# Performance work log

Measured on AMD Instinct MI355X. Metric: run time of the kernel, lower is better.

The kernel has to match this reference:

```python
import jax, jax.numpy as jnp
import numpy as np
from jax import lax


def _conv(x, W):
    # NCHW conv, stride 1, SAME padding (padding = kernel//2 in original)
    return lax.conv_general_dilated(x, W, (1, 1), 'SAME',
                                    dimension_numbers=('NCHW', 'OIHW', 'NCHW'))


def _cconv(zr, zi, Wr, Wi, br, bi):
    # complex conv: (zr + i*zi) * (Wr + i*Wi)
    yr = _conv(zr, Wr) - _conv(zi, Wi) + br[None, :, None, None]
    yi = _conv(zr, Wi) + _conv(zi, Wr) + bi[None, :, None, None]
    return yr, yi


def setup_inputs() -> dict:
    key = jax.random.key(0)
    B, C, H, W = 16, 128, 64, 64        # C = 128 total = 64 real + 64 imag channels
    half = C // 2                        # 64 complex channels
    kin = (C + C) // 2                   # (input+hidden)/2 complex input channels = 128
    K = 3
    ks = jax.random.split(key, 20)
    inp = {
        'x':      jax.random.normal(ks[0], (B, C, H, W), jnp.float32),
        'h_prev': jax.random.normal(ks[1], (B, C, H, W), jnp.float32),
        'c_prev': jax.random.normal(ks[2], (B, C, H, W), jnp.float32),
    }
    i = 3
    for g in ('i', 'f', 'o', 'c'):
        inp['Wr_' + g] = jax.random.normal(ks[i], (half, kin, K, K), jnp.float32) * 0.05; i += 1
        inp['Wi_' + g] = jax.random.normal(ks[i], (half, kin, K, K), jnp.float32) * 0.05; i += 1
        inp['br_' + g] = jax.random.normal(ks[i], (half,), jnp.float32) * 0.05; i += 1
        inp['bi_' + g] = jax.random.normal(ks[i], (half,), jnp.float32) * 0.05; i += 1
    return inp


def reference(x, h_prev, c_prev,
              Wr_i, Wi_i, br_i, bi_i,
              Wr_f, Wi_f, br_f, bi_f,
              Wr_o, Wi_o, br_o, bi_o,
              Wr_c, Wi_c, br_c, bi_c):
    C = x.shape[1]
    h = C // 2
    xr, xi = x[:, :h], x[:, h:]
    hr, hi = h_prev[:, :h], h_prev[:, h:]
    cr, ci = c_prev[:, :h], c_prev[:, h:]

    zr = jnp.concatenate([xr, hr], axis=1)   # real part of combined
    zi = jnp.concatenate([xi, hi], axis=1)   # imag part of combined

    # gates: complex conv then split sigmoid / tanh (applied per component)
    i_r, i_i = map(jax.nn.sigmoid, _cconv(zr, zi, Wr_i, Wi_i, br_i, bi_i))
    # f gate conv output is computed but unused in final update (original bug keeps x as f)
    o_r, o_i = map(jax.nn.sigmoid, _cconv(zr, zi, Wr_o, Wi_o, br_o, bi_o))
    ct_r, ct_i = map(jnp.tanh, _cconv(zr, zi, Wr_c, Wi_c, br_c, bi_c))

    # faithful to original: f_r/f_i taken from x, not from conv_f output
    c_new_r = xr * cr - xi * ci + i_r * ct_r - i_i * ct_i
    c_new_i = xr * ci + xi * cr + i_r * ct_i + i_i * ct_r

    t_r = jnp.tanh(c_new_r)
    t_i = jnp.tanh(c_new_i)
    h_new = jnp.concatenate([o_r * t_r - o_i * t_i, o_r * t_i + o_i * t_r], axis=1)
    c_new = jnp.concatenate([c_new_r, c_new_i], axis=1)
    return h_new, c_new
```

## Files before the change

### kernel.cpp

```cpp
#include <hip/hip_runtime.h>
#include <hip/hip_bf16.h>


typedef __attribute__((ext_vector_type(8))) short short8;
typedef __attribute__((ext_vector_type(4))) float floatx4;
typedef __attribute__((ext_vector_type(4))) float float4v;

#define MTOT   65536
#define HSIZE  8388608

__device__ __forceinline__ short f2bf(float f) {
  __hip_bfloat16 h = __float2bfloat16(f);
  return *reinterpret_cast<short*>(&h);
}

__device__ __forceinline__ float bf2f(short s) {
  unsigned u = ((unsigned)(unsigned short)s) << 16;
  return __uint_as_float(u);
}

__device__ __forceinline__ void gload16(const short* g, void* lds) {
  __builtin_amdgcn_global_load_lds(
      (__attribute__((address_space(1))) void*)(g),
      (__attribute__((address_space(3))) void*)(lds), 16, 0, 0);
}

__global__ __launch_bounds__(256) void halo_zero_kernel(short* __restrict__ Zp) {
  int t = blockIdx.x * 256 + threadIdx.x;
  int s   = t & 31;
  int pix = t >> 5;
  int b = pix / 260;
  int r = pix - b * 260;
  int yp, xp;
  if (r < 66)       { yp = 0;               xp = r; }
  else if (r < 132) { yp = 65;              xp = r - 66; }
  else { int r2 = r - 132; yp = 1 + (r2 >> 1); xp = (r2 & 1) * 65; }
  short8 z;
#pragma unroll
  for (int q = 0; q < 8; ++q) z[q] = 0;
  *(short8*)(Zp + (((b * 66 + yp) * 66 + xp) * 256 + s * 8)) = z;
}

__global__ __launch_bounds__(256) void pack_z_kernel(
    const float* __restrict__ xs, const float* __restrict__ hs,
    short* __restrict__ Zp) {
  __shared__ short tile[64 * 72];
  int bid = blockIdx.x;
  int y      = bid & 63;
  int half   = (bid >> 6) & 1;
  int srcSel = (bid >> 7) & 1;
  int b      = bid >> 8;
  const float* src = srcSel ? hs : xs;
  int chBase  = half * 64;
  int cinBase = half * 128 + srcSel * 64;
  int t = threadIdx.x;
  int x4 = t & 15, chq = t >> 4;
#pragma unroll
  for (int p = 0; p < 4; ++p) {
    int ch = p * 16 + chq;
    float4v f = *(const float4v*)(src + (size_t)(b * 128 + chBase + ch) * 4096 + y * 64 + x4 * 4);
#pragma unroll
    for (int e = 0; e < 4; ++e)
      tile[(x4 * 4 + e) * 72 + ch] = f2bf(f[e]);
  }
  __syncthreads();
  int x = t >> 2, seg = t & 3;
  short8 v0 = *(const short8*)(tile + x * 72 + seg * 16);
  short8 v1 = *(const short8*)(tile + x * 72 + seg * 16 + 8);
  size_t outp = ((size_t)(b * 66 + y + 1) * 66 + x + 1) * 256 + cinBase + seg * 16;
  *(short8*)(Zp + outp)     = v0;
  *(short8*)(Zp + outp + 8) = v1;
}

__global__ __launch_bounds__(256) void pack_w_kernel(
    const float* __restrict__ Wr_i, const float* __restrict__ Wi_i,
    const float* __restrict__ Wr_o, const float* __restrict__ Wi_o,
    const float* __restrict__ Wr_c, const float* __restrict__ Wi_c,
    const float* __restrict__ br_i, const float* __restrict__ bi_i,
    const float* __restrict__ br_o, const float* __restrict__ bi_o,
    const float* __restrict__ br_c, const float* __restrict__ bi_c,
    short* __restrict__ Wp, float* __restrict__ bias) {
  int g = blockIdx.x * 256 + threadIdx.x;
  if (g >= 384 * 9 * 256) return;
  int cin = g & 255;
  int tap = (g >> 8) % 9;
  int n   = g / (256 * 9);
  int part = n >> 6, ch = n & 63;
  const float *Wr, *Wi;
  if (part < 2)      { Wr = Wr_i; Wi = Wi_i; }
  else if (part < 4) { Wr = Wr_o; Wi = Wi_o; }
  else               { Wr = Wr_c; Wi = Wi_c; }
  int im = part & 1;
  int ci = cin & 127;
  int second = cin >> 7;
  const float* src = im ? (second ? Wr : Wi) : (second ? Wi : Wr);
  float f = src[(ch * 128 + ci) * 9 + tap];
  if (!im && second) f = -f;
  Wp[(n * 9 + tap) * 256 + cin] = f2bf(f);
  if (g < 384) {
    int p2 = g >> 6, c2 = g & 63;
    const float* bs = (p2 == 0) ? br_i : (p2 == 1) ? bi_i : (p2 == 2) ? br_o
                    : (p2 == 3) ? bi_o : (p2 == 4) ? br_c : bi_c;
    bias[g] = bs[c2];
  }
}

__device__ __forceinline__ void issueA(const short* __restrict__ Wp, int n0,
                                       int ta, int dxa, short8* dst, int tid, int wv) {
  int dy  = ta >> 2;
  int c0  = (ta & 3) * 64;
  int tap = dy * 3 + dxa;
#pragma unroll
  for (int it = 0; it < 4; ++it) {
    int idx = tid + it * 256;
    int row = idx >> 3, p = idx & 7;
    int g = p ^ (row & 7);
    gload16(Wp + ((size_t)((n0 + row) * 9 + tap) * 256 + c0 + g * 8),
            (void*)(dst + (it * 256 + wv * 64)));
  }
}

__device__ __forceinline__ void issueB(const short* __restrict__ Z, int zrow0,
                                       int tb, short8* dst, int tid, int wv) {
  int dy = tb >> 2;
  int c0 = (tb & 3) * 64;
#pragma unroll
  for (int it = 0; it < 4; ++it) {
    int idx = tid + it * 256;
    int r2  = idx >> 9;
    int rem = idx & 511;
    int col = (rem >> 3) + 1;
    int p   = rem & 7;
    int g   = p ^ (col & 7);
    int ygl = zrow0 + dy + r2;
    int idx0 = it * 256 + wv * 64;
    int r2d  = idx0 >> 9;
    int rem0 = idx0 & 511;
    gload16(Z + ((size_t)(ygl * 66 + col) * 256 + c0 + g * 8),
            (void*)(dst + (r2d * 528 + 8 + rem0)));
  }
}

template<int DXI>
__device__ __forceinline__ void compute_step(const short8* __restrict__ Ac,
                                             const short8* __restrict__ Bc,
                                             floatx4 (&acc)[4][4],
                                             int wch, int r2w, int l15, int l4) {
#pragma unroll
  for (int kk = 0; kk < 2; ++kk) {
    int kg = kk * 4 + l4;
    short8 a[4], bv[4];
#pragma unroll
    for (int i = 0; i < 4; ++i) {
      int row = wch + i * 16 + l15;
      a[i] = Ac[row * 8 + (kg ^ (row & 7))];
    }
#pragma unroll
    for (int j = 0; j < 4; ++j) {
      int col = j * 16 + l15 + DXI;
      bv[j] = Bc[r2w * 528 + col * 8 + (kg ^ (col & 7))];
    }
#pragma unroll
    for (int i = 0; i < 4; ++i)
#pragma unroll
      for (int j = 0; j < 4; ++j)
        acc[i][j] = __builtin_amdgcn_mfma_f32_16x16x32_bf16(a[i], bv[j], acc[i][j], 0, 0, 0);
  }
}

__global__ __launch_bounds__(256, 2) void conv_gemm(
    const short* __restrict__ Z, const short* __restrict__ Wp,
    const float* __restrict__ bias, __hip_bfloat16* __restrict__ gates) {
  __shared__ short8 As[2][1024];
  __shared__ short8 Bs[2][1056];

  const int tid = threadIdx.x;
  const int wv = tid >> 6, lane = tid & 63;
  const int l15 = lane & 15, l4 = lane >> 4;
  const int m0 = blockIdx.x * 128;
  const int n0 = blockIdx.y * 128;
  const int b  = m0 >> 12;
  const int y0 = (m0 >> 6) & 63;
  const int zrow0 = b * 66 + y0;
  const int wch = (wv & 1) * 64;
  const int r2w = wv >> 1;

  floatx4 acc[4][4];
#pragma unroll
  for (int i = 0; i < 4; ++i)
#pragma unroll
    for (int j = 0; j < 4; ++j)
#pragma unroll
      for (int r = 0; r < 4; ++r) acc[i][j][r] = 0.f;

  if (tid < 64) {
    int buf = tid >> 5, w = tid & 31;
    int r2 = w >> 4, hi = (w >> 3) & 1, p = w & 7;
    short8 z;
#pragma unroll
    for (int q = 0; q < 8; ++q) z[q] = 0;
    Bs[buf][r2 * 528 + (hi ? 520 : 0) + p] = z;
  }
  issueA(Wp, n0, 0, 0, &As[0][0], tid, wv);
  issueB(Z, zrow0, 0, &Bs[0][0], tid, wv);
  asm volatile("s_waitcnt lgkmcnt(0)" ::: "memory");

#define CONV_STEP(NW, DXI, DOA, TA, DXA, ADST, DOB, TB, BDST, AC, BC)          \
  do {                                                                         \
    if (DOA) issueA(Wp, n0, (TA), (DXA), &As[ADST][0], tid, wv);               \
    if (DOB) issueB(Z, zrow0, (TB), &Bs[BDST][0], tid, wv);                    \
    asm volatile("s_waitcnt vmcnt(" #NW ")" ::: "memory");                     \
    __builtin_amdgcn_sched_barrier(0);                                         \
    __builtin_amdgcn_s_barrier();                                              \
    __builtin_amdgcn_sched_barrier(0);                                         \
    __builtin_amdgcn_s_setprio(1);                                             \
    compute_step<DXI>(&As[AC][0], &Bs[BC][0], acc, wch, r2w, l15, l4);         \
    __builtin_amdgcn_s_setprio(0);                                             \
    __builtin_amdgcn_sched_barrier(0);                                         \
    __builtin_amdgcn_s_barrier();                                              \
    __builtin_amdgcn_sched_barrier(0);                                         \
  } while (0)

  for (int tt = 0; tt < 5; ++tt) {
    int t0 = tt * 2;
    CONV_STEP(8, 0, true, t0,     1, 1, true,  t0 + 1, 1, 0, 0);
    CONV_STEP(8, 1, true, t0,     2, 0, false, 0,      0, 1, 0);
    CONV_STEP(4, 2, true, t0 + 1, 0, 1, false, 0,      0, 0, 0);
    CONV_STEP(8, 0, true, t0 + 1, 1, 0, true,  t0 + 2, 0, 1, 1);
    CONV_STEP(8, 1, true, t0 + 1, 2, 1, false, 0,      0, 0, 1);
    CONV_STEP(4, 2, true, t0 + 2, 0, 0, false, 0,      0, 1, 1);
  }
  CONV_STEP(8, 0, true, 10, 1, 1, true,  11, 1, 0, 0);
  CONV_STEP(8, 1, true, 10, 2, 0, false, 0,  0, 1, 0);
  CONV_STEP(4, 2, true, 11, 0, 1, false, 0,  0, 0, 0);
  CONV_STEP(4, 0, true, 11, 1, 0, false, 0,  0, 1, 1);
  CONV_STEP(4, 1, true, 11, 2, 1, false, 0,  0, 0, 1);
  CONV_STEP(0, 2, false, 0, 0, 0, false, 0,  0, 1, 1);
#undef CONV_STEP

#pragma unroll
  for (int i = 0; i < 4; ++i)
#pragma unroll
    for (int j = 0; j < 4; ++j)
#pragma unroll
      for (int r = 0; r < 4; ++r) {
        int ch = n0 + wch + i * 16 + l4 * 4 + r;
        int px = m0 + r2w * 64 + j * 16 + l15;
        gates[(size_t)ch * MTOT + px] = __float2bfloat16(acc[i][j][r] + bias[ch]);
      }
}

__device__ __forceinline__ float fsig(float v) { return 1.f / (1.f + __expf(-v)); }
__device__ __forceinline__ float ftanh(float v) {
  float e = __expf(2.f * v);
  return 1.f - 2.f / (e + 1.f);
}

__global__ __launch_bounds__(256) void epilogue_kernel(
    const __hip_bfloat16* __restrict__ gates,
    const float* __restrict__ x,
    const float* __restrict__ c_prev,
    float* __restrict__ out) {
  int t = blockIdx.x * 256 + threadIdx.x;
  int ch = t >> 13;
  int m  = (t & 8191) << 3;
  int b = m >> 12, sp = m & 4095;

  size_t gbase = (size_t)ch * MTOT + m;
  short8 gri = *(const short8*)((const short*)gates + gbase);
  short8 gii = *(const short8*)((const short*)gates + gbase + (size_t)64 * MTOT);
  short8 gro = *(const short8*)((const short*)gates + gbase + (size_t)128 * MTOT);
  short8 gio = *(const short8*)((const short*)gates + gbase + (size_t)192 * MTOT);
  short8 grc = *(const short8*)((const short*)gates + gbase + (size_t)256 * MTOT);
  short8 gic = *(const short8*)((const short*)gates + gbase + (size_t)320 * MTOT);

  int base = (b * 128 + ch) * 4096 + sp;
  float xr[8] __attribute__((aligned(16)));
  float xi[8] __attribute__((aligned(16)));
  float cr[8] __attribute__((aligned(16)));
  float ci[8] __attribute__((aligned(16)));
  *(float4v*)(xr)     = *(const float4v*)(x + base);
  *(float4v*)(xr + 4) = *(const float4v*)(x + base + 4);
  *(float4v*)(xi)     = *(const float4v*)(x + base + 64 * 4096);
  *(float4v*)(xi + 4) = *(const float4v*)(x + base + 64 * 4096 + 4);
  *(float4v*)(cr)     = *(const float4v*)(c_prev + base);
  *(float4v*)(cr + 4) = *(const float4v*)(c_prev + base + 4);
  *(float4v*)(ci)     = *(const float4v*)(c_prev + base + 64 * 4096);
  *(float4v*)(ci + 4) = *(const float4v*)(c_prev + base + 64 * 4096 + 4);

  float hr[8] __attribute__((aligned(16)));
  float hi[8] __attribute__((aligned(16)));
  float nr[8] __attribute__((aligned(16)));
  float ni[8] __attribute__((aligned(16)));
#pragma unroll
  for (int q = 0; q < 8; ++q) {
    float i_r = fsig(bf2f(gri[q])), i_i = fsig(bf2f(gii[q]));
    float o_r = fsig(bf2f(gro[q])), o_i = fsig(bf2f(gio[q]));
    float ct_r = ftanh(bf2f(grc[q])), ct_i = ftanh(bf2f(gic[q]));
    float cnr = xr[q] * cr[q] - xi[q] * ci[q] + i_r * ct_r - i_i * ct_i;
    float cni = xr[q] * ci[q] + xi[q] * cr[q] + i_r * ct_i + i_i * ct_r;
    float tr = ftanh(cnr), ti = ftanh(cni);
    hr[q] = o_r * tr - o_i * ti;
    hi[q] = o_r * ti + o_i * tr;
    nr[q] = cnr;
    ni[q] = cni;
  }

  *(float4v*)(out + base)                         = *(const float4v*)(hr);
  *(float4v*)(out + base + 4)                     = *(const float4v*)(hr + 4);
  *(float4v*)(out + base + 64 * 4096)             = *(const float4v*)(hi);
  *(float4v*)(out + base + 64 * 4096 + 4)         = *(const float4v*)(hi + 4);
  *(float4v*)(out + HSIZE + base)                 = *(const float4v*)(nr);
  *(float4v*)(out + HSIZE + base + 4)             = *(const float4v*)(nr + 4);
  *(float4v*)(out + HSIZE + base + 64 * 4096)     = *(const float4v*)(ni);
  *(float4v*)(out + HSIZE + base + 64 * 4096 + 4) = *(const float4v*)(ni + 4);
}

extern "C" void kernel_launch(void* const* d_in, const int* in_sizes, int n_in,
                              void* d_out, int out_size, void* d_ws, size_t ws_size,
                              hipStream_t stream) {
  const float* x = (const float*)d_in[0];
  const float* h = (const float*)d_in[1];

  char* ws = (char*)d_ws;
  short* Zp   = (short*)ws;
  short* Wp   = (short*)(ws + 35684352);
  float* bias = (float*)(ws + 37453824);
  __hip_bfloat16* gates = (__hip_bfloat16*)(ws + 37455360);

  halo_zero_kernel<<<520, 256, 0, stream>>>(Zp);
  pack_z_kernel<<<4096, 256, 0, stream>>>(x, h, Zp);
  pack_w_kernel<<<3456, 256, 0, stream>>>(
      (const float*)d_in[3], (const float*)d_in[4],
      (const float*)d_in[11], (const float*)d_in[12],
      (const float*)d_in[15], (const float*)d_in[16],
      (const float*)d_in[5], (const float*)d_in[6],
      (const float*)d_in[13], (const float*)d_in[14],
      (const float*)d_in[17], (const float*)d_in[18],
      Wp, bias);
  conv_gemm<<<dim3(512, 3), 256, 0, stream>>>(Zp, Wp, bias, gates);
  epilogue_kernel<<<2048, 256, 0, stream>>>(
      gates, (const float*)d_in[0], (const float*)d_in[2],
      (float*)d_out);
}
```

Before: 318.2 us.

## Software-pipeline LDS fragment reads with MFMA and halve barriers per step

Splits each conv step into two k-halves. The second half's fragments are read from LDS while the first half's MFMAs run, and the next step's first-half fragments are prefetched after the barrier. Global loads are now issued after the single per-step barrier rather than before it, which removes one of the two barriers per step. This costs extra registers for the double fragment sets and needs more complex buffer-index bookkeeping, so a wrong index could corrupt results.

```diff
diff --git a/kernel.cpp b/kernel.cpp
--- a/kernel.cpp
+++ b/kernel.cpp
@@ -141,31 +141,31 @@
   }
 }
 
-template<int DXI>
-__device__ __forceinline__ void compute_step(const short8* __restrict__ Ac,
-                                             const short8* __restrict__ Bc,
-                                             floatx4 (&acc)[4][4],
-                                             int wch, int r2w, int l15, int l4) {
-#pragma unroll
-  for (int kk = 0; kk < 2; ++kk) {
-    int kg = kk * 4 + l4;
-    short8 a[4], bv[4];
-#pragma unroll
-    for (int i = 0; i < 4; ++i) {
-      int row = wch + i * 16 + l15;
-      a[i] = Ac[row * 8 + (kg ^ (row & 7))];
-    }
-#pragma unroll
-    for (int j = 0; j < 4; ++j) {
-      int col = j * 16 + l15 + DXI;
-      bv[j] = Bc[r2w * 528 + col * 8 + (kg ^ (col & 7))];
-    }
-#pragma unroll
-    for (int i = 0; i < 4; ++i)
-#pragma unroll
-      for (int j = 0; j < 4; ++j)
-        acc[i][j] = __builtin_amdgcn_mfma_f32_16x16x32_bf16(a[i], bv[j], acc[i][j], 0, 0, 0);
-  }
+template<int KK, int DXI>
+__device__ __forceinline__ void frag_read(const short8* __restrict__ Ab,
+                                          const short8* __restrict__ Bb,
+                                          short8 (&a)[4], short8 (&bv)[4],
+                                          int wch, int r2w, int l15, int l4) {
+  int kg = KK * 4 + l4;
+#pragma unroll
+  for (int i = 0; i < 4; ++i) {
+    int row = wch + i * 16 + l15;
+    a[i] = Ab[row * 8 + (kg ^ (row & 7))];
+  }
+#pragma unroll
+  for (int j = 0; j < 4; ++j) {
+    int col = j * 16 + l15 + DXI;
+    bv[j] = Bb[r2w * 528 + col * 8 + (kg ^ (col & 7))];
+  }
+}
+
+__device__ __forceinline__ void mfma16(const short8 (&a)[4], const short8 (&bv)[4],
+                                       floatx4 (&acc)[4][4]) {
+#pragma unroll
+  for (int i = 0; i < 4; ++i)
+#pragma unroll
+    for (int j = 0; j < 4; ++j)
+      acc[i][j] = __builtin_amdgcn_mfma_f32_16x16x32_bf16(a[i], bv[j], acc[i][j], 0, 0, 0);
 }
 
 __global__ __launch_bounds__(256, 2) void conv_gemm(
@@ -193,6 +193,8 @@
 #pragma unroll
       for (int r = 0; r < 4; ++r) acc[i][j][r] = 0.f;
 
+  short8 af0[4], bf0[4], af1[4], bf1[4];
+
   if (tid < 64) {
     int buf = tid >> 5, w = tid & 31;
     int r2 = w >> 4, hi = (w >> 3) & 1, p = w & 7;
@@ -203,40 +205,53 @@
   }
   issueA(Wp, n0, 0, 0, &As[0][0], tid, wv);
   issueB(Z, zrow0, 0, &Bs[0][0], tid, wv);
-  asm volatile("s_waitcnt lgkmcnt(0)" ::: "memory");
-
-#define CONV_STEP(NW, DXI, DOA, TA, DXA, ADST, DOB, TB, BDST, AC, BC)          \
+  issueA(Wp, n0, 0, 1, &As[1][0], tid, wv);
+  __builtin_amdgcn_sched_barrier(0);
+  asm volatile("s_waitcnt vmcnt(4) lgkmcnt(0)" ::: "memory");
+  __builtin_amdgcn_sched_barrier(0);
+  __builtin_amdgcn_s_barrier();
+  __builtin_amdgcn_sched_barrier(0);
+  frag_read<0, 0>(&As[0][0], &Bs[0][0], af0, bf0, wch, r2w, l15, l4);
+
+#define STEP(NW, DOA, TOA, DXA, ABUF, DOB, TOB, BISS, TBUF, TBN, ANXT, DXS, DXN, DON) \
   do {                                                                         \
-    if (DOA) issueA(Wp, n0, (TA), (DXA), &As[ADST][0], tid, wv);               \
-    if (DOB) issueB(Z, zrow0, (TB), &Bs[BDST][0], tid, wv);                    \
-    asm volatile("s_waitcnt vmcnt(" #NW ")" ::: "memory");                     \
+    frag_read<1, DXS>(&As[ABUF][0], &Bs[TBUF][0], af1, bf1, wch, r2w, l15, l4);\
+    __builtin_amdgcn_s_setprio(1);                                             \
+    mfma16(af0, bf0, acc);                                                     \
+    __builtin_amdgcn_s_setprio(0);                                             \
+    __builtin_amdgcn_sched_barrier(0);                                         \
+    asm volatile("s_waitcnt vmcnt(" #NW ") lgkmcnt(0)" ::: "memory");          \
     __builtin_amdgcn_sched_barrier(0);                                         \
     __builtin_amdgcn_s_barrier();                                              \
     __builtin_amdgcn_sched_barrier(0);                                         \
+    if (DOA) issueA(Wp, n0, t0 + (TOA), (DXA), &As[ABUF][0], tid, wv);         \
+    if (DOB) issueB(Z, zrow0, t0 + (TOB), &Bs[BISS][0], tid, wv);              \
+    if (DON) frag_read<0, DXN>(&As[ANXT][0], &Bs[TBN][0], af0, bf0,            \
+                               wch, r2w, l15, l4);                             \
     __builtin_amdgcn_s_setprio(1);                                             \
-    compute_step<DXI>(&As[AC][0], &Bs[BC][0], acc, wch, r2w, l15, l4);         \
+    mfma16(af1, bf1, acc);                                                     \
     __builtin_amdgcn_s_setprio(0);                                             \
-    __builtin_amdgcn_sched_barrier(0);                                         \
-    __builtin_amdgcn_s_barrier();                                              \
-    __builtin_amdgcn_sched_barrier(0);                                         \
   } while (0)
 
-  for (int tt = 0; tt < 5; ++tt) {
-    int t0 = tt * 2;
-    CONV_STEP(8, 0, true, t0,     1, 1, true,  t0 + 1, 1, 0, 0);
-    CONV_STEP(8, 1, true, t0,     2, 0, false, 0,      0, 1, 0);
-    CONV_STEP(4, 2, true, t0 + 1, 0, 1, false, 0,      0, 0, 0);
-    CONV_STEP(8, 0, true, t0 + 1, 1, 0, true,  t0 + 2, 0, 1, 1);
-    CONV_STEP(8, 1, true, t0 + 1, 2, 1, false, 0,      0, 0, 1);
-    CONV_STEP(4, 2, true, t0 + 2, 0, 0, false, 0,      0, 1, 1);
-  }
-  CONV_STEP(8, 0, true, 10, 1, 1, true,  11, 1, 0, 0);
-  CONV_STEP(8, 1, true, 10, 2, 0, false, 0,  0, 1, 0);
-  CONV_STEP(4, 2, true, 11, 0, 1, false, 0,  0, 0, 0);
-  CONV_STEP(4, 0, true, 11, 1, 0, false, 0,  0, 1, 1);
-  CONV_STEP(4, 1, true, 11, 2, 1, false, 0,  0, 0, 1);
-  CONV_STEP(0, 2, false, 0, 0, 0, false, 0,  0, 1, 1);
-#undef CONV_STEP
+  for (int u = 0; u < 5; ++u) {
+    int t0 = u * 2;
+    STEP(0,  1,  0,  2,  0,   1,  1,  1,   0,   0,  1,   0,  1,  1);
+    STEP(4,  1,  1,  0,  1,   0,  0,  0,   0,   0,  0,   1,  2,  1);
+    STEP(0,  1,  1,  1,  0,   0,  0,  0,   0,   1,  1,   2,  0,  1);
+    STEP(0,  1,  1,  2,  1,   1,  2,  0,   1,   1,  0,   0,  1,  1);
+    STEP(4,  1,  2,  0,  0,   0,  0,  0,   1,   1,  1,   1,  2,  1);
+    STEP(0,  1,  2,  1,  1,   0,  0,  0,   1,   0,  0,   2,  0,  1);
+  }
+  {
+    int t0 = 10;
+    STEP(0,  1,  0,  2,  0,   1,  1,  1,   0,   0,  1,   0,  1,  1);
+    STEP(4,  1,  1,  0,  1,   0,  0,  0,   0,   0,  0,   1,  2,  1);
+    STEP(0,  1,  1,  1,  0,   0,  0,  0,   0,   1,  1,   2,  0,  1);
+    STEP(0,  1,  1,  2,  1,   0,  0,  0,   1,   1,  0,   0,  1,  1);
+    STEP(0,  0,  0,  0,  0,   0,  0,  0,   1,   1,  1,   1,  2,  1);
+    STEP(0,  0,  0,  0,  1,   0,  0,  0,   1,   0,  0,   2,  0,  0);
+  }
+#undef STEP
 
 #pragma unroll
   for (int i = 0; i < 4; ++i)
```

After: 317.9 us. No clear change (-0.1%).
